# Kernel tuning notes

Measured on AMD Instinct MI355X. Metric: run time of the kernel, lower is better.

The kernel has to match this reference:

```python
import jax, jax.numpy as jnp
import numpy as np

B = 1
Z, H, W = 8, 48, 180
C = 384
HEADS = 12
WS = (2, 6, 10)  # window size (z, h, w)
N = WS[0] * WS[1] * WS[2]          # 120 tokens per window
NW = (Z // WS[0]) * (H // WS[1]) * (W // WS[2])  # 576 windows
BIAS_ROWS = (2 * WS[2] - 1) * WS[1] * WS[1] * WS[0] * WS[0]  # 2736


def _position_index(ws):
    w0, w1, w2 = ws
    zi = np.arange(w0); zj = -np.arange(w0) * w0
    hi = np.arange(w1); hj = -np.arange(w1) * w1
    ww = np.arange(w2)
    c1 = np.stack(np.meshgrid(zi, hi, ww, indexing='ij')).reshape(3, -1)
    c2 = np.stack(np.meshgrid(zj, hj, ww, indexing='ij')).reshape(3, -1)
    coords = (c1[:, :, None] - c2[:, None, :]).transpose(1, 2, 0).copy()  # (N, N, 3)
    coords[:, :, 2] += w2 - 1
    coords[:, :, 1] *= 2 * w2 - 1
    coords[:, :, 0] *= (2 * w2 - 1) * w1 * w1
    return jnp.asarray(coords.sum(-1).reshape(-1), dtype=jnp.int32)  # (N*N,)

POS_IDX = _position_index(WS)


def setup_inputs() -> dict:
    key = jax.random.key(0)
    ks = jax.random.split(key, 16)
    s = 0.02
    return {
        'x': jax.random.normal(ks[0], (B, Z * H * W, C), dtype=jnp.float32),
        'wqkv': jax.random.normal(ks[1], (C, 3 * C), dtype=jnp.float32) * s,
        'bqkv': jnp.zeros((3 * C,), dtype=jnp.float32),
        'wproj': jax.random.normal(ks[2], (C, C), dtype=jnp.float32) * s,
        'bproj': jnp.zeros((C,), dtype=jnp.float32),
        'bias_table': jax.random.normal(ks[3], (BIAS_ROWS, NW, HEADS), dtype=jnp.float32) * s,
        'g1': jnp.ones((C,), dtype=jnp.float32),
        'b1': jnp.zeros((C,), dtype=jnp.float32),
        'g2': jnp.ones((C,), dtype=jnp.float32),
        'b2': jnp.zeros((C,), dtype=jnp.float32),
        'wm1': jax.random.normal(ks[4], (C, 4 * C), dtype=jnp.float32) * s,
        'bm1': jnp.zeros((4 * C,), dtype=jnp.float32),
        'wm2': jax.random.normal(ks[5], (4 * C, C), dtype=jnp.float32) * s,
        'bm2': jnp.zeros((C,), dtype=jnp.float32),
    }


def _layernorm(x, g, b, eps=1e-5):
    mu = jnp.mean(x, axis=-1, keepdims=True)
    var = jnp.var(x, axis=-1, keepdims=True)
    return (x - mu) * jax.lax.rsqrt(var + eps) * g + b


def _block(x, wqkv, bqkv, wproj, bproj, bias_table, g1, b1, g2, b2, wm1, bm1, wm2, bm2):
    w0, w1, w2 = WS
    d = C // HEADS
    scale = d ** -0.5
    shortcut = x
    xr = x.reshape(B, Z, H, W, C)
    # window_partition -> (B*nW, N, C)
    xw = xr.reshape(B, Z // w0, w0, H // w1, w1, W // w2, w2, C)
    xw = xw.transpose(0, 1, 3, 5, 2, 4, 6, 7).reshape(-1, N, C)
    # qkv projection, split heads: (3, B*nW, heads, N, d)
    qkv = (xw @ wqkv + bqkv).reshape(-1, N, 3, HEADS, d).transpose(2, 0, 3, 1, 4)
    q, k, v = qkv[0], qkv[1], qkv[2]
    attn = jnp.einsum('whnd,whmd->whnm', q * scale, k)  # (B*nW, heads, N, N)
    # earth-specific bias: gather + reshape to (nW, heads, N, N)
    bias = bias_table[POS_IDX].reshape(N, N, NW, HEADS).transpose(2, 3, 0, 1)
    attn = jax.nn.softmax(attn + bias, axis=-1)
    out = jnp.einsum('whnm,whmd->whnd', attn, v)
    # NOTE: source reshapes (B*nW, heads, N, d) -> (B*nW, N, C) directly (no transpose)
    out = out.reshape(-1, N, C)
    out = out @ wproj + bproj
    # window_reverse -> (B, Z*H*W, C)
    xr = out.reshape(B, Z // w0, H // w1, W // w2, w0, w1, w2, C)
    xr = xr.transpose(0, 1, 4, 2, 5, 3, 6, 7).reshape(B, Z * H * W, C)
    x = shortcut + _layernorm(xr, g1, b1)
    # MLP with post-norm residual
    h = jax.nn.gelu(x @ wm1 + bm1, approximate=False)
    m = h @ wm2 + bm2
    return x + _layernorm(m, g2, b2)


def reference(x, wqkv, bqkv, wproj, bproj, bias_table, g1, b1, g2, b2, wm1, bm1, wm2, bm2):
    return _block(x, wqkv, bqkv, wproj, bproj, bias_table, g1, b1, g2, b2, wm1, bm1, wm2, bm2)
```

## Files before the change

### kernel.cpp

```cpp
#include <hip/hip_runtime.h>
#include <math.h>

#define L_TOK 69120
#define C_DIM 384
#define C3 1152
#define C4 1536
#define N_TOK 120
#define N_HEAD 12
#define BIAS_ROWS 2736
#define WH 6912
#define CHUNK 13824
#define NCHUNK 5

typedef __attribute__((ext_vector_type(8))) short short8;
typedef __attribute__((ext_vector_type(4))) float floatx4;

__device__ __forceinline__ unsigned short f2bf(float f) {
    union { float f; unsigned int u; } c; c.f = f;
    unsigned int u = c.u;
    return (unsigned short)((u + 0x7fffu + ((u >> 16) & 1u)) >> 16);
}
__device__ __forceinline__ float bf2f(unsigned short s) {
    union { unsigned int u; float f; } c; c.u = ((unsigned int)s) << 16;
    return c.f;
}

__device__ __forceinline__ void gl_lds16(const void* g, void* l) {
    __builtin_amdgcn_global_load_lds((const __attribute__((address_space(1))) unsigned int*)g,
                                     (__attribute__((address_space(3))) unsigned int*)l, 16, 0, 0);
}

__device__ __forceinline__ void xcd_swz(int gx, int nwg, int* bx, int* by) {
    int orig = blockIdx.y * gx + blockIdx.x;
    int q8 = nwg >> 3, r8 = nwg & 7;
    int xcd = orig & 7, lin = orig >> 3;
    int sw = (xcd < r8 ? xcd * (q8 + 1) : r8 * (q8 + 1) + (xcd - r8) * q8) + lin;
    *bx = sw % gx;
    *by = sw / gx;
}

__device__ __forceinline__ int win_to_global(int m) {
    int w_idx = m / N_TOK;
    int n = m - w_idx * N_TOK;
    int zw = w_idx / 144;
    int rem = w_idx - zw * 144;
    int hw = rem / 18;
    int ww = rem - hw * 18;
    int zl = n / 60;
    int r2 = n - zl * 60;
    int hl = r2 / 10;
    int wl = r2 - hl * 10;
    return ((zw * 2 + zl) * 48 + hw * 6 + hl) * 180 + ww * 10 + wl;
}

__global__ __launch_bounds__(256) void k_wt(const float* __restrict__ W,
                                            unsigned short* __restrict__ WT, int K, int N, int perm) {
    __shared__ float tle[32][33];
    int n0 = blockIdx.x << 5, k0 = blockIdx.y << 5;
    for (int i = threadIdx.y; i < 32; i += 8) {
        int n = n0 + threadIdx.x;
        int src = perm ? ((n & ~63) | ((n & 15) << 2) | ((n >> 4) & 3)) : n;
        tle[i][threadIdx.x] = W[(size_t)(k0 + i) * N + src];
    }
    __syncthreads();
    for (int i = threadIdx.y; i < 32; i += 8)
        WT[(size_t)(n0 + i) * K + k0 + threadIdx.x] = f2bf(tle[threadIdx.x][i]);
}

__global__ __launch_bounds__(256) void k_bt(const float* __restrict__ Bsrc,
                                            unsigned short* __restrict__ BTt) {
    __shared__ float tle[32][33];
    int c0 = blockIdx.x << 5;
    int r0 = blockIdx.y << 5;
    for (int i = threadIdx.y; i < 32; i += 8) {
        int r = r0 + i;
        if (r < BIAS_ROWS) tle[i][threadIdx.x] = Bsrc[(size_t)r * WH + c0 + threadIdx.x];
    }
    __syncthreads();
    int rr = r0 + threadIdx.x;
    if (rr < BIAS_ROWS)
        for (int i = threadIdx.y; i < 32; i += 8)
            BTt[(size_t)(c0 + i) * BIAS_ROWS + rr] = f2bf(tle[threadIdx.x][i]);
}

__global__ __launch_bounds__(256) void k_xc(const float* __restrict__ x,
                                            unsigned short* __restrict__ xb) {
    int gid = blockIdx.x * 256 + threadIdx.x;
    int m = gid / 48;
    int seg = gid - m * 48;
    const float* src = x + (size_t)win_to_global(m) * C_DIM + seg * 8;
    float4 a = *(const float4*)(src);
    float4 b = *(const float4*)(src + 4);
    uint4 o;
    o.x = (unsigned int)f2bf(a.x) | ((unsigned int)f2bf(a.y) << 16);
    o.y = (unsigned int)f2bf(a.z) | ((unsigned int)f2bf(a.w) << 16);
    o.z = (unsigned int)f2bf(b.x) | ((unsigned int)f2bf(b.y) << 16);
    o.w = (unsigned int)f2bf(b.z) | ((unsigned int)f2bf(b.w) << 16);
    *(uint4*)(xb + (size_t)m * C_DIM + seg * 8) = o;
}

template <int K>
__device__ __forceinline__ void mfma_loop(const unsigned short* __restrict__ A,
                                          const unsigned short* __restrict__ BT,
                                          unsigned short* As, unsigned short* Bs,
                                          int m0, int n0, floatx4 acc[4][4]) {
    const int tid = threadIdx.x;
    const int wave = tid >> 6, lane = tid & 63;
    const int wm = (wave >> 1) << 6, wn = (wave & 1) << 6;
    const int lm = lane & 15, lq = lane >> 4;
    const int srow = lane >> 2, scol = (lane & 3) << 3;
    const unsigned short* ags = A + (size_t)(m0 + wave * 32 + srow) * K + scol;
    const unsigned short* bgs = BT + (size_t)(n0 + wave * 32 + srow) * K + scol;
    char* lA = (char*)As + wave * 2048;
    char* lB = (char*)Bs + wave * 2048;
    for (int kk = 0; kk < K; kk += 32) {
        gl_lds16(ags + kk, lA);
        gl_lds16(ags + (size_t)16 * K + kk, lA + 1024);
        gl_lds16(bgs + kk, lB);
        gl_lds16(bgs + (size_t)16 * K + kk, lB + 1024);
        __syncthreads();
        short8 af[4], bq[4];
#pragma unroll
        for (int i = 0; i < 4; ++i) af[i] = *(const short8*)(As + (wm + i * 16 + lm) * 32 + lq * 8);
#pragma unroll
        for (int j = 0; j < 4; ++j) bq[j] = *(const short8*)(Bs + (wn + j * 16 + lm) * 32 + lq * 8);
#pragma unroll
        for (int i = 0; i < 4; ++i)
#pragma unroll
            for (int j = 0; j < 4; ++j)
                acc[i][j] = __builtin_amdgcn_mfma_f32_16x16x32_bf16(af[i], bq[j], acc[i][j], 0, 0, 0);
        __syncthreads();
    }
}

__global__ __launch_bounds__(256) void k_qkv(const unsigned short* __restrict__ xb,
                                             const unsigned short* __restrict__ wqkvT,
                                             const float* __restrict__ bqkv,
                                             unsigned short* __restrict__ q,
                                             unsigned short* __restrict__ kbuf,
                                             unsigned short* __restrict__ vbuf) {
    __shared__ __align__(16) unsigned short smem[128 * 136];
    unsigned short* As = smem;
    unsigned short* Bs = smem + 128 * 32;
    const int tid = threadIdx.x;
    int bx, by;
    xcd_swz(9, 9 * (L_TOK / 128), &bx, &by);
    const int m0 = by << 7, n0 = bx << 7;
    const int wave = tid >> 6, lane = tid & 63;
    const int wm = (wave >> 1) << 6, wn = (wave & 1) << 6;
    const int lm = lane & 15, lq = lane >> 4;

    floatx4 acc[4][4];
#pragma unroll
    for (int i = 0; i < 4; ++i)
#pragma unroll
        for (int j = 0; j < 4; ++j) acc[i][j] = (floatx4){0.f, 0.f, 0.f, 0.f};
    mfma_loop<C_DIM>(xb, wqkvT, As, Bs, m0, n0, acc);

    const int sel = bx / 3;
    unsigned short* dst = (sel == 0) ? q : (sel == 1) ? kbuf : vbuf;
    const float scl = (sel == 0) ? 0.17677669529663687f : 1.0f;
    float4 b4 = *(const float4*)(bqkv + n0 + wn + 4 * lm);

    if (sel < 2) {
#pragma unroll
        for (int i = 0; i < 4; ++i)
#pragma unroll
            for (int r = 0; r < 4; ++r) {
                uint2 pk;
                pk.x = (unsigned int)f2bf((acc[i][0][r] + b4.x) * scl) |
                       ((unsigned int)f2bf((acc[i][1][r] + b4.y) * scl) << 16);
                pk.y = (unsigned int)f2bf((acc[i][2][r] + b4.z) * scl) |
                       ((unsigned int)f2bf((acc[i][3][r] + b4.w) * scl) << 16);
                *(uint2*)(smem + (wm + i * 16 + lq * 4 + r) * 136 + wn + 4 * lm) = pk;
            }
        __syncthreads();
#pragma unroll
        for (int it = 0; it < 8; ++it) {
            int s = it * 256 + tid;
            int row = s >> 4, cs = (s & 15) << 3;
            uint4 vv = *(const uint4*)(smem + row * 136 + cs);
            int m = m0 + row;
            int wi = m / N_TOK, nn = m - wi * N_TOK;
            int c2 = n0 + cs - sel * C_DIM;
            int head = c2 >> 5, dd = c2 & 31;
            *(uint4*)(dst + (((size_t)(wi * N_HEAD + head) * N_TOK + nn) << 5) + dd) = vv;
        }
    } else {
#pragma unroll
        for (int i = 0; i < 4; ++i)
#pragma unroll
            for (int j = 0; j < 4; ++j) {
                float bj = (j == 0) ? b4.x : (j == 1) ? b4.y : (j == 2) ? b4.z : b4.w;
                uint2 pk;
                pk.x = (unsigned int)f2bf(acc[i][j][0] + bj) |
                       ((unsigned int)f2bf(acc[i][j][1] + bj) << 16);
                pk.y = (unsigned int)f2bf(acc[i][j][2] + bj) |
                       ((unsigned int)f2bf(acc[i][j][3] + bj) << 16);
                *(uint2*)(smem + (wn + 4 * lm + j) * 136 + wm + i * 16 + lq * 4) = pk;
            }
        __syncthreads();
#pragma unroll
        for (int it = 0; it < 8; ++it) {
            int s = it * 256 + tid;
            int c = s >> 4, mo = (s & 15) << 3;
            uint4 vv = *(const uint4*)(smem + c * 136 + mo);
            int m = m0 + mo;
            int wi = m / N_TOK, nn = m - wi * N_TOK;
            int c2 = n0 + c - 2 * C_DIM;
            int head = c2 >> 5, dd = c2 & 31;
            *(uint4*)(dst + ((size_t)(wi * N_HEAD + head) * 32 + dd) * N_TOK + nn) = vv;
        }
    }
}

__global__ __launch_bounds__(256) void k_attn(const unsigned short* __restrict__ q,
                                              const unsigned short* __restrict__ k,
                                              const unsigned short* __restrict__ vt,
                                              const unsigned short* __restrict__ btabT,
                                              unsigned short* __restrict__ ao) {
    const int wh = blockIdx.x;
    const int w = wh / N_HEAD;
    const int h = wh - w * N_HEAD;
    __shared__ float blds[BIAS_ROWS];
    __shared__ __align__(16) unsigned short plds[4][16 * 136];
    const int tid = threadIdx.x;
    const unsigned short* bptr = btabT + (size_t)wh * BIAS_ROWS;
    for (int i = tid; i < BIAS_ROWS; i += 256) blds[i] = bf2f(bptr[i]);
    __syncthreads();

    const int wave = tid >> 6, lane = tid & 63;
    const int lm = lane & 15, lq = lane >> 4;
    const unsigned short* kwh = k + (size_t)wh * N_TOK * 32;
    const unsigned short* qwh = q + (size_t)wh * N_TOK * 32;
    const unsigned short* vwh = vt + (size_t)wh * 32 * N_TOK;
    unsigned short* pl = plds[wave];

    short8 kfr[8];
#pragma unroll
    for (int kt = 0; kt < 8; ++kt)
        kfr[kt] = *(const short8*)(kwh + (size_t)(kt * 16 + lm) * 32 + lq * 8);

    int p0v[8], d2v[8], d3v[8];
#pragma unroll
    for (int kt = 0; kt < 8; ++kt) {
        int k0 = kt * 16 + lq * 4;
        int z2 = (k0 >= 60) ? 1 : 0;
        int k0m = k0 - 60 * z2;
        int h2 = k0m / 10;
        int w2 = k0m - 10 * h2;
        p0v[kt] = z2 * 1368 + h2 * 114 - w2;
        d2v[kt] = (w2 == 8) ? 122 : -2;
        d3v[kt] = (w2 == 8) ? 121 : -3;
    }

    for (int qi = 0; qi < 2; ++qi) {
        const int qt = wave + 4 * qi;
        short8 qfr = *(const short8*)(qwh + (size_t)(qt * 16 + lm) * 32 + lq * 8);
        floatx4 sc[8];
#pragma unroll
        for (int kt = 0; kt < 8; ++kt)
            sc[kt] = __builtin_amdgcn_mfma_f32_16x16x32_bf16(kfr[kt], qfr,
                                                             (floatx4){0.f, 0.f, 0.f, 0.f}, 0, 0, 0);
        int qg = qt * 16 + lm;
        int zl = qg / 60;
        int r2 = qg - zl * 60;
        int hl = r2 / 10;
        int wl = r2 - hl * 10;
        int pbase = zl * 684 + hl * 19 + wl + 9;
        pbase = min(pbase, 797);
#pragma unroll
        for (int kt = 0; kt < 8; ++kt) {
            if (kt == 7 && lq >= 2) {
                sc[kt] = (floatx4){-1e30f, -1e30f, -1e30f, -1e30f};
            } else {
                int base = pbase + p0v[kt];
                sc[kt][0] += blds[base];
                sc[kt][1] += blds[base - 1];
                sc[kt][2] += blds[base + d2v[kt]];
                sc[kt][3] += blds[base + d3v[kt]];
            }
        }
        float mx = -1e30f;
#pragma unroll
        for (int kt = 0; kt < 8; ++kt)
#pragma unroll
            for (int r = 0; r < 4; ++r) mx = fmaxf(mx, sc[kt][r]);
        mx = fmaxf(mx, __shfl_xor(mx, 16, 64));
        mx = fmaxf(mx, __shfl_xor(mx, 32, 64));
        float l = 0.f;
#pragma unroll
        for (int kt = 0; kt < 8; ++kt)
#pragma unroll
            for (int r = 0; r < 4; ++r) {
                float p = __expf(sc[kt][r] - mx);
                sc[kt][r] = p;
                l += p;
            }
        l += __shfl_xor(l, 16, 64);
        l += __shfl_xor(l, 32, 64);
        float inv = 1.f / l;
#pragma unroll
        for (int kt = 0; kt < 8; ++kt) {
            uint2 pk;
            pk.x = (unsigned int)f2bf(sc[kt][0] * inv) | ((unsigned int)f2bf(sc[kt][1] * inv) << 16);
            pk.y = (unsigned int)f2bf(sc[kt][2] * inv) | ((unsigned int)f2bf(sc[kt][3] * inv) << 16);
            *(uint2*)(pl + lm * 136 + kt * 16 + lq * 4) = pk;
        }
        floatx4 oac[2] = {(floatx4){0.f, 0.f, 0.f, 0.f}, (floatx4){0.f, 0.f, 0.f, 0.f}};
#pragma unroll
        for (int ks = 0; ks < 4; ++ks) {
            short8 af = *(const short8*)(pl + lm * 136 + ks * 32 + lq * 8);
#pragma unroll
            for (int ct = 0; ct < 2; ++ct) {
                short8 bf = *(const short8*)(vwh + (size_t)(ct * 16 + lm) * N_TOK + ks * 32 + lq * 8);
                oac[ct] = __builtin_amdgcn_mfma_f32_16x16x32_bf16(af, bf, oac[ct], 0, 0, 0);
            }
        }
#pragma unroll
        for (int r = 0; r < 4; ++r) {
            int qg2 = qt * 16 + lq * 4 + r;
            if (qg2 < N_TOK) {
                int rq = qg2 / 12;
                int rr = h * 10 + rq;
                int cc = (qg2 - rq * 12) * 32;
#pragma unroll
                for (int ct = 0; ct < 2; ++ct)
                    ao[((size_t)w * N_TOK + rr) * C_DIM + cc + ct * 16 + lm] = f2bf(oac[ct][r]);
            }
        }
    }
}

__global__ __launch_bounds__(256) void k_proj(const unsigned short* __restrict__ ao,
                                              const unsigned short* __restrict__ wprojT,
                                              const float* __restrict__ bproj,
                                              float* __restrict__ p) {
    __shared__ unsigned short As[128 * 32];
    __shared__ unsigned short Bs[128 * 32];
    const int tid = threadIdx.x;
    const int wave = tid >> 6, lane = tid & 63;
    const int wm = (wave >> 1) << 6, wn = (wave & 1) << 6;
    const int lm = lane & 15, lq = lane >> 4;
    int bx, by;
    xcd_swz(3, 3 * (L_TOK / 128), &bx, &by);
    const int m0 = by << 7, n0 = bx << 7;
    floatx4 acc[4][4];
#pragma unroll
    for (int i = 0; i < 4; ++i)
#pragma unroll
        for (int j = 0; j < 4; ++j) acc[i][j] = (floatx4){0.f, 0.f, 0.f, 0.f};
    mfma_loop<C_DIM>(ao, wprojT, As, Bs, m0, n0, acc);
#pragma unroll
    for (int i = 0; i < 4; ++i) {
        int rowb = m0 + wm + i * 16 + lq * 4;
        int gg[4];
#pragma unroll
        for (int r = 0; r < 4; ++r) gg[r] = win_to_global(rowb + r);
#pragma unroll
        for (int j = 0; j < 4; ++j) {
            int colg = n0 + wn + j * 16 + lm;
            float bias = bproj[colg];
#pragma unroll
            for (int r = 0; r < 4; ++r)
                p[(size_t)gg[r] * C_DIM + colg] = acc[i][j][r] + bias;
        }
    }
}

__global__ __launch_bounds__(256) void k_mlp1(const unsigned short* __restrict__ x1b,
                                              const unsigned short* __restrict__ wm1T,
                                              const float* __restrict__ bm1,
                                              unsigned short* __restrict__ hbuf) {
    __shared__ __align__(16) unsigned short smem[128 * 136];
    unsigned short* As = smem;
    unsigned short* Bs = smem + 128 * 32;
    const int tid = threadIdx.x;
    const int wave = tid >> 6, lane = tid & 63;
    const int wm = (wave >> 1) << 6, wn = (wave & 1) << 6;
    const int lm = lane & 15, lq = lane >> 4;
    int bx, by;
    xcd_swz(12, 12 * (CHUNK / 128), &bx, &by);
    const int m0 = by << 7, n0 = bx << 7;
    floatx4 acc[4][4];
#pragma unroll
    for (int i = 0; i < 4; ++i)
#pragma unroll
        for (int j = 0; j < 4; ++j) acc[i][j] = (floatx4){0.f, 0.f, 0.f, 0.f};
    mfma_loop<C_DIM>(x1b, wm1T, As, Bs, m0, n0, acc);

    float4 b4 = *(const float4*)(bm1 + n0 + wn + 4 * lm);
#pragma unroll
    for (int i = 0; i < 4; ++i)
#pragma unroll
        for (int r = 0; r < 4; ++r) {
            float v0 = acc[i][0][r] + b4.x;
            float v1 = acc[i][1][r] + b4.y;
            float v2 = acc[i][2][r] + b4.z;
            float v3 = acc[i][3][r] + b4.w;
            v0 = 0.5f * v0 * (1.f + erff(v0 * 0.70710678118654752f));
            v1 = 0.5f * v1 * (1.f + erff(v1 * 0.70710678118654752f));
            v2 = 0.5f * v2 * (1.f + erff(v2 * 0.70710678118654752f));
            v3 = 0.5f * v3 * (1.f + erff(v3 * 0.70710678118654752f));
            uint2 pk;
            pk.x = (unsigned int)f2bf(v0) | ((unsigned int)f2bf(v1) << 16);
            pk.y = (unsigned int)f2bf(v2) | ((unsigned int)f2bf(v3) << 16);
            *(uint2*)(smem + (wm + i * 16 + lq * 4 + r) * 136 + wn + 4 * lm) = pk;
        }
    __syncthreads();
#pragma unroll
    for (int it = 0; it < 8; ++it) {
        int s = it * 256 + tid;
        int row = s >> 4, cs = (s & 15) << 3;
        uint4 vv = *(const uint4*)(smem + row * 136 + cs);
        *(uint4*)(hbuf + (size_t)(m0 + row) * C4 + n0 + cs) = vv;
    }
}

__global__ __launch_bounds__(256) void k_mlp2(const unsigned short* __restrict__ hbuf,
                                              const unsigned short* __restrict__ wm2T,
                                              const float* __restrict__ bm2,
                                              float* __restrict__ mbuf) {
    __shared__ unsigned short As[128 * 32];
    __shared__ unsigned short Bs[128 * 32];
    const int tid = threadIdx.x;
    const int wave = tid >> 6, lane = tid & 63;
    const int wm = (wave >> 1) << 6, wn = (wave & 1) << 6;
    const int lm = lane & 15, lq = lane >> 4;
    int bx, by;
    xcd_swz(3, 3 * (CHUNK / 128), &bx, &by);
    const int m0 = by << 7, n0 = bx << 7;
    floatx4 acc[4][4];
#pragma unroll
    for (int i = 0; i < 4; ++i)
#pragma unroll
        for (int j = 0; j < 4; ++j) acc[i][j] = (floatx4){0.f, 0.f, 0.f, 0.f};
    mfma_loop<C4>(hbuf, wm2T, As, Bs, m0, n0, acc);
#pragma unroll
    for (int i = 0; i < 4; ++i) {
        int rowb = m0 + wm + i * 16 + lq * 4;
#pragma unroll
        for (int j = 0; j < 4; ++j) {
            int colg = n0 + wn + j * 16 + lm;
            float bias = bm2[colg];
#pragma unroll
            for (int r = 0; r < 4; ++r)
                mbuf[(size_t)(rowb + r) * C_DIM + colg] = acc[i][j][r] + bias;
        }
    }
}

__global__ __launch_bounds__(128) void k_ln_res(const float* __restrict__ src,
                                                const float* __restrict__ resid,
                                                const float* __restrict__ gamma,
                                                const float* __restrict__ beta,
                                                float* __restrict__ outp,
                                                unsigned short* __restrict__ out_bf) {
    const int row = blockIdx.x;
    const int t = threadIdx.x;
    const float* sr = src + (size_t)row * C_DIM;
    float v0 = sr[t], v1 = sr[t + 128], v2 = sr[t + 256];
    __shared__ float rs[128], rq[128];
    rs[t] = v0 + v1 + v2;
    rq[t] = v0 * v0 + v1 * v1 + v2 * v2;
    __syncthreads();
    for (int off = 64; off > 0; off >>= 1) {
        if (t < off) { rs[t] += rs[t + off]; rq[t] += rq[t + off]; }
        __syncthreads();
    }
    float mu = rs[0] * (1.f / 384.f);
    float var = rq[0] * (1.f / 384.f) - mu * mu;
    float rinv = rsqrtf(var + 1e-5f);
    const float* rr = resid + (size_t)row * C_DIM;
    float* orow = outp + (size_t)row * C_DIM;
    float y0 = rr[t]       + (v0 - mu) * rinv * gamma[t]       + beta[t];
    float y1 = rr[t + 128] + (v1 - mu) * rinv * gamma[t + 128] + beta[t + 128];
    float y2 = rr[t + 256] + (v2 - mu) * rinv * gamma[t + 256] + beta[t + 256];
    orow[t] = y0; orow[t + 128] = y1; orow[t + 256] = y2;
    if (out_bf) {
        unsigned short* ob = out_bf + (size_t)row * C_DIM;
        ob[t] = f2bf(y0); ob[t + 128] = f2bf(y1); ob[t + 256] = f2bf(y2);
    }
}

extern "C" void kernel_launch(void* const* d_in, const int* in_sizes, int n_in,
                              void* d_out, int out_size, void* d_ws, size_t ws_size,
                              hipStream_t stream) {
    const float* x     = (const float*)d_in[0];
    const float* wqkv  = (const float*)d_in[1];
    const float* bqkv  = (const float*)d_in[2];
    const float* wproj = (const float*)d_in[3];
    const float* bproj = (const float*)d_in[4];
    const float* btab  = (const float*)d_in[5];
    const float* g1    = (const float*)d_in[6];
    const float* b1    = (const float*)d_in[7];
    const float* g2    = (const float*)d_in[8];
    const float* b2    = (const float*)d_in[9];
    const float* wm1   = (const float*)d_in[10];
    const float* bm1   = (const float*)d_in[11];
    const float* wm2   = (const float*)d_in[12];
    const float* bm2   = (const float*)d_in[13];
    float* outp = (float*)d_out;

    const size_t LC = (size_t)L_TOK * C_DIM;
    if (ws_size < 8 * LC) return;
    char* ws = (char*)d_ws;
    const size_t QB = LC * 2;
    unsigned short* qb  = (unsigned short*)ws;
    unsigned short* kb  = (unsigned short*)(ws + QB);
    unsigned short* vb  = (unsigned short*)(ws + 2 * QB);
    unsigned short* btT = (unsigned short*)(ws + 3 * QB);
    unsigned short* hbuf = (unsigned short*)(ws + 3 * QB);
    size_t wof = 3 * QB + (size_t)CHUNK * C4 * 2;
    unsigned short* wqkvT = (unsigned short*)(ws + wof);
    unsigned short* wprojT = wqkvT + (size_t)C3 * C_DIM;
    unsigned short* wm1T   = wprojT + (size_t)C_DIM * C_DIM;
    unsigned short* wm2T   = wm1T + (size_t)C_DIM * C4;
    unsigned short* aob = qb;
    float* proj = (float*)(ws + QB);
    float* x1   = proj;
    unsigned short* x1b = qb;
    unsigned short* xbuf = (unsigned short*)d_out;

    dim3 tb(32, 8);
    k_wt<<<dim3(C3 / 32, C_DIM / 32), tb, 0, stream>>>(wqkv, wqkvT, C_DIM, C3, 1);
    k_wt<<<dim3(C_DIM / 32, C_DIM / 32), tb, 0, stream>>>(wproj, wprojT, C_DIM, C_DIM, 0);
    k_wt<<<dim3(C4 / 32, C_DIM / 32), tb, 0, stream>>>(wm1, wm1T, C_DIM, C4, 1);
    k_wt<<<dim3(C_DIM / 32, C4 / 32), tb, 0, stream>>>(wm2, wm2T, C4, C_DIM, 0);
    k_bt<<<dim3(WH / 32, (BIAS_ROWS + 31) / 32), tb, 0, stream>>>(btab, btT);

    k_xc<<<dim3(L_TOK * 48 / 256), dim3(256), 0, stream>>>(x, xbuf);
    k_qkv<<<dim3(C3 / 128, L_TOK / 128), dim3(256), 0, stream>>>(xbuf, wqkvT, bqkv, qb, kb, vb);
    k_attn<<<dim3(WH), dim3(256), 0, stream>>>(qb, kb, vb, btT, aob);
    k_proj<<<dim3(C_DIM / 128, L_TOK / 128), dim3(256), 0, stream>>>(aob, wprojT, bproj, proj);
    k_ln_res<<<dim3(L_TOK), dim3(128), 0, stream>>>(proj, x, g1, b1, x1, x1b);
    for (int c = 0; c < NCHUNK; ++c) {
        size_t r0 = (size_t)c * CHUNK;
        float* mbuf = outp + r0 * C_DIM;
        k_mlp1<<<dim3(C4 / 128, CHUNK / 128), dim3(256), 0, stream>>>(x1b + r0 * C_DIM, wm1T, bm1, hbuf);
        k_mlp2<<<dim3(C_DIM / 128, CHUNK / 128), dim3(256), 0, stream>>>(hbuf, wm2T, bm2, mbuf);
        k_ln_res<<<dim3(CHUNK), dim3(128), 0, stream>>>(mbuf, x1 + r0 * C_DIM, g2, b2, mbuf, (unsigned short*)nullptr);
    }
    (void)in_sizes; (void)n_in; (void)out_size;
}
```

Measured before the change: 1.089 ms.

## Double-buffer GEMM LDS tiles and streamline attention softmax and output stores

The shared GEMM mainloop now double-buffers its A/B tiles in LDS, prefetching the next k-slice with global_load_lds while the current one feeds MFMAs, so only one barrier per iteration is needed. The attention kernel uses exp2 with a pre-scaled max, packs to bf16 with the hardware v_cvt_pk_bf16_f32 instruction, and defers the 1/l normalization to the PV output. Attention outputs are staged in LDS and written with coalesced 16-byte stores instead of scattered 2-byte stores. Costs are doubled LDS for the GEMM buffers, extra LDS in attention, and slightly different rounding because P is left unnormalized in bf16.

```diff
diff --git a/kernel.cpp b/kernel.cpp
--- a/kernel.cpp
+++ b/kernel.cpp
@@ -23,6 +23,11 @@
 __device__ __forceinline__ float bf2f(unsigned short s) {
     union { unsigned int u; float f; } c; c.u = ((unsigned int)s) << 16;
     return c.f;
+}
+__device__ __forceinline__ unsigned int cvtpk_bf16(float lo, float hi) {
+    unsigned int r;
+    asm("v_cvt_pk_bf16_f32 %0, %1, %2" : "=v"(r) : "v"(lo), "v"(hi));
+    return r;
 }
 
 __device__ __forceinline__ void gl_lds16(const void* g, void* l) {
@@ -102,7 +107,7 @@
 template <int K>
 __device__ __forceinline__ void mfma_loop(const unsigned short* __restrict__ A,
                                           const unsigned short* __restrict__ BT,
-                                          unsigned short* As, unsigned short* Bs,
+                                          unsigned short* S,
                                           int m0, int n0, floatx4 acc[4][4]) {
     const int tid = threadIdx.x;
     const int wave = tid >> 6, lane = tid & 63;
@@ -111,14 +116,30 @@
     const int srow = lane >> 2, scol = (lane & 3) << 3;
     const unsigned short* ags = A + (size_t)(m0 + wave * 32 + srow) * K + scol;
     const unsigned short* bgs = BT + (size_t)(n0 + wave * 32 + srow) * K + scol;
-    char* lA = (char*)As + wave * 2048;
-    char* lB = (char*)Bs + wave * 2048;
-    for (int kk = 0; kk < K; kk += 32) {
-        gl_lds16(ags + kk, lA);
-        gl_lds16(ags + (size_t)16 * K + kk, lA + 1024);
-        gl_lds16(bgs + kk, lB);
-        gl_lds16(bgs + (size_t)16 * K + kk, lB + 1024);
-        __syncthreads();
+    constexpr int NK = K / 32;
+    {
+        char* lA = (char*)S + wave * 2048;
+        char* lB = (char*)(S + 4096) + wave * 2048;
+        gl_lds16(ags, lA);
+        gl_lds16(ags + (size_t)16 * K, lA + 1024);
+        gl_lds16(bgs, lB);
+        gl_lds16(bgs + (size_t)16 * K, lB + 1024);
+    }
+    __syncthreads();
+#pragma unroll 2
+    for (int t = 0; t < NK; ++t) {
+        if (t + 1 < NK) {
+            const int nxt = (t + 1) & 1;
+            const int kk = (t + 1) * 32;
+            char* lA = (char*)(S + nxt * 8192) + wave * 2048;
+            char* lB = (char*)(S + nxt * 8192 + 4096) + wave * 2048;
+            gl_lds16(ags + kk, lA);
+            gl_lds16(ags + (size_t)16 * K + kk, lA + 1024);
+            gl_lds16(bgs + kk, lB);
+            gl_lds16(bgs + (size_t)16 * K + kk, lB + 1024);
+        }
+        const unsigned short* As = S + (t & 1) * 8192;
+        const unsigned short* Bs = As + 4096;
         short8 af[4], bq[4];
 #pragma unroll
         for (int i = 0; i < 4; ++i) af[i] = *(const short8*)(As + (wm + i * 16 + lm) * 32 + lq * 8);
@@ -140,8 +161,6 @@
                                              unsigned short* __restrict__ kbuf,
                                              unsigned short* __restrict__ vbuf) {
     __shared__ __align__(16) unsigned short smem[128 * 136];
-    unsigned short* As = smem;
-    unsigned short* Bs = smem + 128 * 32;
     const int tid = threadIdx.x;
     int bx, by;
     xcd_swz(9, 9 * (L_TOK / 128), &bx, &by);
@@ -155,7 +174,7 @@
     for (int i = 0; i < 4; ++i)
 #pragma unroll
         for (int j = 0; j < 4; ++j) acc[i][j] = (floatx4){0.f, 0.f, 0.f, 0.f};
-    mfma_loop<C_DIM>(xb, wqkvT, As, Bs, m0, n0, acc);
+    mfma_loop<C_DIM>(xb, wqkvT, smem, m0, n0, acc);
 
     const int sel = bx / 3;
     unsigned short* dst = (sel == 0) ? q : (sel == 1) ? kbuf : vbuf;
@@ -224,6 +243,7 @@
     const int h = wh - w * N_HEAD;
     __shared__ float blds[BIAS_ROWS];
     __shared__ __align__(16) unsigned short plds[4][16 * 136];
+    __shared__ __align__(16) unsigned short oq[120 * 40];
     const int tid = threadIdx.x;
     const unsigned short* bptr = btabT + (size_t)wh * BIAS_ROWS;
     for (int i = tid; i < BIAS_ROWS; i += 256) blds[i] = bf2f(bptr[i]);
@@ -288,12 +308,13 @@
             for (int r = 0; r < 4; ++r) mx = fmaxf(mx, sc[kt][r]);
         mx = fmaxf(mx, __shfl_xor(mx, 16, 64));
         mx = fmaxf(mx, __shfl_xor(mx, 32, 64));
+        const float mxs = mx * 1.44269504f;
         float l = 0.f;
 #pragma unroll
         for (int kt = 0; kt < 8; ++kt)
 #pragma unroll
             for (int r = 0; r < 4; ++r) {
-                float p = __expf(sc[kt][r] - mx);
+                float p = exp2f(fmaf(sc[kt][r], 1.44269504f, -mxs));
                 sc[kt][r] = p;
                 l += p;
             }
@@ -303,8 +324,8 @@
 #pragma unroll
         for (int kt = 0; kt < 8; ++kt) {
             uint2 pk;
-            pk.x = (unsigned int)f2bf(sc[kt][0] * inv) | ((unsigned int)f2bf(sc[kt][1] * inv) << 16);
-            pk.y = (unsigned int)f2bf(sc[kt][2] * inv) | ((unsigned int)f2bf(sc[kt][3] * inv) << 16);
+            pk.x = cvtpk_bf16(sc[kt][0], sc[kt][1]);
+            pk.y = cvtpk_bf16(sc[kt][2], sc[kt][3]);
             *(uint2*)(pl + lm * 136 + kt * 16 + lq * 4) = pk;
         }
         floatx4 oac[2] = {(floatx4){0.f, 0.f, 0.f, 0.f}, (floatx4){0.f, 0.f, 0.f, 0.f}};
@@ -319,16 +340,24 @@
         }
 #pragma unroll
         for (int r = 0; r < 4; ++r) {
+            float ir = __shfl(inv, lq * 4 + r, 16);
             int qg2 = qt * 16 + lq * 4 + r;
             if (qg2 < N_TOK) {
-                int rq = qg2 / 12;
-                int rr = h * 10 + rq;
-                int cc = (qg2 - rq * 12) * 32;
-#pragma unroll
-                for (int ct = 0; ct < 2; ++ct)
-                    ao[((size_t)w * N_TOK + rr) * C_DIM + cc + ct * 16 + lm] = f2bf(oac[ct][r]);
+                unsigned int u = cvtpk_bf16(oac[0][r] * ir, oac[1][r] * ir);
+                oq[qg2 * 40 + lm] = (unsigned short)u;
+                oq[qg2 * 40 + 16 + lm] = (unsigned short)(u >> 16);
             }
         }
+    }
+    __syncthreads();
+    const size_t obase = ((size_t)w * N_TOK + h * 10) * C_DIM;
+    for (int idx = tid; idx < 480; idx += 256) {
+        int o0 = idx << 3;
+        int rq = o0 / 384;
+        int c = o0 - rq * 384;
+        int ql = c >> 5, d0 = c & 31;
+        uint4 vv = *(const uint4*)(oq + (rq * 12 + ql) * 40 + d0);
+        *(uint4*)(ao + obase + o0) = vv;
     }
 }
 
@@ -336,8 +365,7 @@
                                               const unsigned short* __restrict__ wprojT,
                                               const float* __restrict__ bproj,
                                               float* __restrict__ p) {
-    __shared__ unsigned short As[128 * 32];
-    __shared__ unsigned short Bs[128 * 32];
+    __shared__ __align__(16) unsigned short S[16384];
     const int tid = threadIdx.x;
     const int wave = tid >> 6, lane = tid & 63;
     const int wm = (wave >> 1) << 6, wn = (wave & 1) << 6;
@@ -350,7 +378,7 @@
     for (int i = 0; i < 4; ++i)
 #pragma unroll
         for (int j = 0; j < 4; ++j) acc[i][j] = (floatx4){0.f, 0.f, 0.f, 0.f};
-    mfma_loop<C_DIM>(ao, wprojT, As, Bs, m0, n0, acc);
+    mfma_loop<C_DIM>(ao, wprojT, S, m0, n0, acc);
 #pragma unroll
     for (int i = 0; i < 4; ++i) {
         int rowb = m0 + wm + i * 16 + lq * 4;
@@ -373,8 +401,6 @@
                                               const float* __restrict__ bm1,
                                               unsigned short* __restrict__ hbuf) {
     __shared__ __align__(16) unsigned short smem[128 * 136];
-    unsigned short* As = smem;
-    unsigned short* Bs = smem + 128 * 32;
     const int tid = threadIdx.x;
     const int wave = tid >> 6, lane = tid & 63;
     const int wm = (wave >> 1) << 6, wn = (wave & 1) << 6;
@@ -387,7 +413,7 @@
     for (int i = 0; i < 4; ++i)
 #pragma unroll
         for (int j = 0; j < 4; ++j) acc[i][j] = (floatx4){0.f, 0.f, 0.f, 0.f};
-    mfma_loop<C_DIM>(x1b, wm1T, As, Bs, m0, n0, acc);
+    mfma_loop<C_DIM>(x1b, wm1T, smem, m0, n0, acc);
 
     float4 b4 = *(const float4*)(bm1 + n0 + wn + 4 * lm);
 #pragma unroll
@@ -421,8 +447,7 @@
                                               const unsigned short* __restrict__ wm2T,
                                               const float* __restrict__ bm2,
                                               float* __restrict__ mbuf) {
-    __shared__ unsigned short As[128 * 32];
-    __shared__ unsigned short Bs[128 * 32];
+    __shared__ __align__(16) unsigned short S[16384];
     const int tid = threadIdx.x;
     const int wave = tid >> 6, lane = tid & 63;
     const int wm = (wave >> 1) << 6, wn = (wave & 1) << 6;
@@ -435,7 +460,7 @@
     for (int i = 0; i < 4; ++i)
 #pragma unroll
         for (int j = 0; j < 4; ++j) acc[i][j] = (floatx4){0.f, 0.f, 0.f, 0.f};
-    mfma_loop<C4>(hbuf, wm2T, As, Bs, m0, n0, acc);
+    mfma_loop<C4>(hbuf, wm2T, S, m0, n0, acc);
 #pragma unroll
     for (int i = 0; i < 4; ++i) {
         int rowb = m0 + wm + i * 16 + lq * 4;
```

Result: faster. 1.057 ms (-3.0%).
